# Kernel optimization log

Hardware: AMD Instinct MI355X
Metric: run time of the kernel (lower is better)

Reference implementation:

```python
import jax, jax.numpy as jnp
import numpy as np

B, H, W, DIM = 8, 128, 128, 96
MED = 2 * DIM            # med_channels
NS = 3                   # num_scales
SCTX = 48                # spatial context channels
RIN = DIM + SCTX         # reweight mlp input
RHID = int(0.25 * RIN)   # 36
ROUT = NS * MED          # 576
FH, FWH = H, W // 2 + 1  # rfft2 output grid
SCALE_HW = [(16, 9), (8, 4), (24, 13)]  # per-scale filter resolutions


def _cubic(t, a=-0.75):
    t = abs(t)
    if t <= 1.0:
        return (a + 2) * t ** 3 - (a + 3) * t ** 2 + 1.0
    if t < 2.0:
        return a * t ** 3 - 5 * a * t ** 2 + 8 * a * t - 4 * a
    return 0.0


def _resize_mat(old, new):
    # bicubic, align_corners=True, border replication (matches F.interpolate)
    M = np.zeros((new, old), dtype=np.float32)
    for j in range(new):
        s = j * (old - 1) / (new - 1) if new > 1 else 0.0
        f = int(np.floor(s))
        for k in range(-1, 3):
            M[j, min(max(f + k, 0), old - 1)] += _cubic(s - (f + k))
    return jnp.asarray(M)


def _soa(x, scale, bias):
    r = jnp.maximum(x, 0.0)
    return scale * r * r + bias


def setup_inputs() -> dict:
    key = jax.random.key(0)
    ks = jax.random.split(key, 10)
    inp = {
        "x": jax.random.normal(ks[0], (B, H, W, DIM), dtype=jnp.float32),
        "w1": jax.random.normal(ks[1], (MED, DIM), dtype=jnp.float32) * 0.02,
        "soa1_scale": jnp.ones((1,), jnp.float32),
        "soa1_bias": jnp.zeros((1,), jnp.float32),
        "cw0": jax.random.normal(ks[2], (SCALE_HW[0][0], SCALE_HW[0][1], MED, 2), dtype=jnp.float32) * 0.02,
        "cw1": jax.random.normal(ks[3], (SCALE_HW[1][0], SCALE_HW[1][1], MED, 2), dtype=jnp.float32) * 0.02,
        "cw2": jax.random.normal(ks[4], (SCALE_HW[2][0], SCALE_HW[2][1], MED, 2), dtype=jnp.float32) * 0.02,
        "sp_w": jax.random.normal(ks[5], (SCTX, DIM), dtype=jnp.float32) * 0.05,
        "bn_gamma": jnp.ones((SCTX,), jnp.float32),
        "bn_beta": jnp.zeros((SCTX,), jnp.float32),
        "bn_mean": jnp.zeros((SCTX,), jnp.float32),
        "bn_var": jnp.ones((SCTX,), jnp.float32),
        "fc1": jax.random.normal(ks[6], (RHID, RIN), dtype=jnp.float32) * 0.05,
        "mlp_scale": jnp.ones((1,), jnp.float32),
        "mlp_bias": jnp.zeros((1,), jnp.float32),
        "fc2": jax.random.normal(ks[7], (ROUT, RHID), dtype=jnp.float32) * 0.05,
        "w2": jax.random.normal(ks[8], (DIM, MED), dtype=jnp.float32) * 0.02,
    }
    return inp


def reference(x, w1, soa1_scale, soa1_bias, cw0, cw1, cw2, sp_w,
              bn_gamma, bn_beta, bn_mean, bn_var,
              fc1, mlp_scale, mlp_bias, fc2, w2):
    # pwconv1 + Soa act
    x_pre = _soa(jnp.einsum('bhwc,mc->bhwm', x, w1), soa1_scale, soa1_bias)
    # rfft2 over spatial dims (ortho) -> [B, FH, FWH, MED] complex64
    xf = jnp.fft.rfft2(x_pre.transpose(0, 3, 1, 2), axes=(2, 3), norm='ortho').transpose(0, 2, 3, 1)
    # resize each scale's complex weight to the fft grid (bicubic align_corners=True)
    filts = []
    for cw in (cw0, cw1, cw2):
        Rh = _resize_mat(cw.shape[0], FH)
        Rw = _resize_mat(cw.shape[1], FWH)
        t = jnp.einsum('Hh,hwmc->Hwmc', Rh, cw)
        t = jnp.einsum('Ww,Hwmc->HWmc', Rw, t)
        filts.append(jax.lax.complex(t[..., 0], t[..., 1]))
    filt = jnp.stack(filts)  # [NS, FH, FWH, MED] complex64
    # routing context: global channel mean + 1x1 conv / BN(eval) / relu / GAP
    gctx = x.mean(axis=(1, 2))  # [B, DIM]
    y = jnp.einsum('bhwc,sc->bhws', x, sp_w)
    y = (y - bn_mean) * jax.lax.rsqrt(bn_var + 1e-5) * bn_gamma + bn_beta
    sctx = jnp.maximum(y, 0.0).mean(axis=(1, 2))  # [B, SCTX]
    fused = jnp.concatenate([gctx, sctx], axis=1)  # [B, RIN]
    hmid = _soa(fused @ fc1.T, mlp_scale, mlp_bias)
    r = jax.nn.softmax((hmid @ fc2.T).reshape(-1, NS, MED), axis=1)  # [B, NS, MED]
    # routing-weighted combined filter + spectral multiply
    comb = jnp.einsum('shwm,bsm->bhwm', filt, r.astype(filt.dtype))
    xff = xf * comb
    xsp = jnp.fft.irfft2(xff.transpose(0, 3, 1, 2), s=(H, W), axes=(2, 3), norm='ortho').transpose(0, 2, 3, 1)
    # act2 is Identity; pwconv2
    return jnp.einsum('bhwm,cm->bhwc', xsp, w2)
```

## Files before the change

kernel.cpp:

```cpp
#include <hip/hip_runtime.h>
#include <math.h>

#define BB    8
#define HH    128
#define WW    128
#define DIM   96
#define MED   192
#define HWPX  16384
#define FWH   65
#define LSTR  67

#define P_OFF     0
#define P_SZ      (8*192*16384)
#define FILT_OFF  (P_OFF + P_SZ)
#define FILT_SZ   (3*192*128*65*2)
#define GS_OFF    (FILT_OFF + FILT_SZ)
#define SS_OFF    (GS_OFF + 768)
#define R_OFF     (SS_OFF + 384)
#define W1B_OFF   (R_OFF + 4608)
#define W2B_OFF   (W1B_OFF + 23040)

typedef __attribute__((ext_vector_type(8))) short short8_t;
typedef __attribute__((ext_vector_type(4))) float float4_t;

__device__ __forceinline__ unsigned short bf16_rne(float f){
  unsigned u = __float_as_uint(f);
  unsigned r = (u + 0x7FFFu + ((u>>16)&1u)) >> 16;
  return (unsigned short)r;
}
__device__ __forceinline__ float bf16_to_f(unsigned short h){
  return __uint_as_float(((unsigned)h) << 16);
}

__global__ __launch_bounds__(256) void k_prep(
    const float* __restrict__ w1, const float* __restrict__ sp_w,
    const float* __restrict__ w2,
    unsigned short* __restrict__ W1B, unsigned short* __restrict__ W2B)
{
  int tid = threadIdx.x + blockIdx.x*256;
  int nthr = 256*36;
  for (int i = tid; i < 2*3*15*512; i += nthr) {
    int j = i & 7, l = (i>>3) & 63;
    int nt = (i>>9) % 15, kc = ((i>>9)/15) % 3, term = i / (3*15*512);
    int r = nt*16 + (l&15);
    int c = kc*32 + (l>>4)*8 + j;
    float v = (r < 192) ? w1[r*96 + c] : sp_w[(r-192)*96 + c];
    unsigned short hi = bf16_rne(v);
    W1B[i] = (term==0) ? hi : bf16_rne(v - bf16_to_f(hi));
  }
  for (int i = tid; i < 2*6*6*512; i += nthr) {
    int j = i & 7, l = (i>>3) & 63;
    int nt = (i>>9) % 6, kc = ((i>>9)/6) % 6, term = i / (6*6*512);
    int cp = nt*16 + (l&15);
    int m  = kc*32 + (l>>4)*8 + j;
    float v = w2[cp*192 + m];
    unsigned short hi = bf16_rne(v);
    W2B[i] = (term==0) ? hi : bf16_rne(v - bf16_to_f(hi));
  }
}

__global__ __launch_bounds__(256) void k_pw1(
    const float* __restrict__ x, const unsigned short* __restrict__ W1B,
    const float* __restrict__ soa_scale, const float* __restrict__ soa_bias,
    const float* __restrict__ bn_gamma, const float* __restrict__ bn_beta,
    const float* __restrict__ bn_mean, const float* __restrict__ bn_var,
    float* __restrict__ P, float* __restrict__ gsum, float* __restrict__ ssum)
{
  __shared__ float red[4][144];
  __shared__ float bnA_s[48], bnB_s[48];
  int t = threadIdx.x;
  int lane = t & 63, wv = t >> 6;
  if (t < 48) {
    float a = bn_gamma[t] * rsqrtf(bn_var[t] + 1e-5f);
    bnA_s[t] = a; bnB_s[t] = bn_beta[t] - bn_mean[t]*a;
  }
  int px0 = blockIdx.x*64 + wv*16;
  int b = (blockIdx.x*64) >> 14;
  int pxl = px0 & 16383;
  int g = lane >> 4;

  float4_t acc[15];
  #pragma unroll
  for (int nt=0; nt<15; ++nt) acc[nt] = (float4_t){0.f,0.f,0.f,0.f};

  #pragma unroll
  for (int kc=0; kc<3; ++kc) {
    const float* xp = x + (size_t)(px0 + (lane&15))*96 + kc*32 + g*8;
    float4 v0 = *(const float4*)xp;
    float4 v1 = *(const float4*)(xp+4);
    float vv[8] = {v0.x,v0.y,v0.z,v0.w, v1.x,v1.y,v1.z,v1.w};
    #pragma unroll
    for (int j=0;j<8;j++){
      float s = vv[j];
      s += __shfl_xor(s, 1);
      s += __shfl_xor(s, 2);
      s += __shfl_xor(s, 4);
      s += __shfl_xor(s, 8);
      if ((lane & 15) == 0) red[wv][kc*32 + g*8 + j] = s;
    }
    short8_t Bh, Bl;
    #pragma unroll
    for (int j=0;j<8;j++){
      unsigned short h = bf16_rne(vv[j]);
      Bh[j] = (short)h;
      Bl[j] = (short)bf16_rne(vv[j] - bf16_to_f(h));
    }
    const short8_t* a_hi = (const short8_t*)(W1B + (size_t)(0*3+kc)*15*512) + lane;
    const short8_t* a_lo = (const short8_t*)(W1B + (size_t)(1*3+kc)*15*512) + lane;
    #pragma unroll
    for (int nt=0; nt<15; ++nt) {
      short8_t Ah = a_hi[nt*64];
      short8_t Al = a_lo[nt*64];
      acc[nt] = __builtin_amdgcn_mfma_f32_16x16x32_bf16(Ah, Bh, acc[nt], 0,0,0);
      acc[nt] = __builtin_amdgcn_mfma_f32_16x16x32_bf16(Ah, Bl, acc[nt], 0,0,0);
      acc[nt] = __builtin_amdgcn_mfma_f32_16x16x32_bf16(Al, Bh, acc[nt], 0,0,0);
    }
  }
  float sc = soa_scale[0], bi = soa_bias[0];
  #pragma unroll
  for (int nt=0; nt<12; ++nt) {
    #pragma unroll
    for (int q=0;q<4;q++){
      float d = acc[nt][q];
      float v = fmaxf(d, 0.f);
      d = sc*v*v + bi;
      int mp = nt*16 + g*4 + q;
      P[(size_t)(b*192 + mp)*HWPX + pxl + (lane&15)] = d;
    }
  }
  #pragma unroll
  for (int tile=0; tile<3; ++tile) {
    #pragma unroll
    for (int q=0;q<4;q++){
      int s = tile*16 + g*4 + q;
      float y = acc[12+tile][q];
      float v = fmaxf(bnA_s[s]*y + bnB_s[s], 0.f);
      v += __shfl_xor(v, 1);
      v += __shfl_xor(v, 2);
      v += __shfl_xor(v, 4);
      v += __shfl_xor(v, 8);
      if ((lane & 15) == 0) red[wv][96 + s] = v;
    }
  }
  __syncthreads();
  if (t < 144) {
    float s = red[0][t] + red[1][t] + red[2][t] + red[3][t];
    if (t < 96) atomicAdd(&gsum[b*96 + t], s);
    else        atomicAdd(&ssum[b*48 + (t-96)], s);
  }
}

__global__ __launch_bounds__(256) void k_pw2(
    const float* __restrict__ P, const unsigned short* __restrict__ W2B,
    float* __restrict__ out)
{
  int t = threadIdx.x;
  int lane = t & 63, wv = t >> 6;
  int px0 = blockIdx.x*64 + wv*16;
  int b = px0 >> 14;
  int pxl = px0 & 16383;

  float4_t acc[6];
  #pragma unroll
  for (int nt=0; nt<6; ++nt) acc[nt] = (float4_t){0.f,0.f,0.f,0.f};

  #pragma unroll
  for (int kc=0; kc<6; ++kc) {
    const float* ap = P + (size_t)(b*192 + kc*32 + (lane>>4)*8)*HWPX + pxl + (lane&15);
    short8_t Ah, Al;
    #pragma unroll
    for (int j=0;j<8;j++){
      float v = ap[(size_t)j*HWPX];
      unsigned short h = bf16_rne(v);
      Ah[j] = (short)h;
      Al[j] = (short)bf16_rne(v - bf16_to_f(h));
    }
    const short8_t* b_hi = (const short8_t*)(W2B + (size_t)(0*6+kc)*6*512) + lane;
    const short8_t* b_lo = (const short8_t*)(W2B + (size_t)(1*6+kc)*6*512) + lane;
    #pragma unroll
    for (int nt=0; nt<6; ++nt) {
      short8_t Bh = b_hi[nt*64];
      short8_t Bl = b_lo[nt*64];
      acc[nt] = __builtin_amdgcn_mfma_f32_16x16x32_bf16(Ah, Bh, acc[nt], 0,0,0);
      acc[nt] = __builtin_amdgcn_mfma_f32_16x16x32_bf16(Ah, Bl, acc[nt], 0,0,0);
      acc[nt] = __builtin_amdgcn_mfma_f32_16x16x32_bf16(Al, Bh, acc[nt], 0,0,0);
    }
  }
  #pragma unroll
  for (int nt=0; nt<6; ++nt) {
    #pragma unroll
    for (int q=0;q<4;q++){
      int px = px0 + (lane>>4)*4 + q;
      out[(size_t)px*96 + nt*16 + (lane&15)] = acc[nt][q];
    }
  }
}

__global__ __launch_bounds__(256) void k_route2(
    const float* __restrict__ gsum, const float* __restrict__ ssum,
    const float* __restrict__ fc1, const float* __restrict__ fc2,
    const float* __restrict__ mlp_scale, const float* __restrict__ mlp_bias,
    float* __restrict__ r_out)
{
  __shared__ float fused[144], hmid[36], rpre[576];
  int t = threadIdx.x, b = blockIdx.x;
  if (t < 96) fused[t] = gsum[b*96+t] * (1.f/16384.f);
  else if (t < 144) fused[t] = ssum[b*48 + (t-96)] * (1.f/16384.f);
  __syncthreads();
  if (t < 36) {
    float a = 0.f;
    for (int i=0;i<144;i++) a = fmaf(fused[i], fc1[t*144+i], a);
    float rr = fmaxf(a, 0.f);
    hmid[t] = mlp_scale[0]*rr*rr + mlp_bias[0];
  }
  __syncthreads();
  for (int o = t; o < 576; o += 256) {
    float a = 0.f;
    for (int j=0;j<36;j++) a = fmaf(hmid[j], fc2[o*36+j], a);
    rpre[o] = a;
  }
  __syncthreads();
  if (t < 192) {
    float v0 = rpre[t], v1 = rpre[192+t], v2 = rpre[384+t];
    float mx = fmaxf(v0, fmaxf(v1, v2));
    float e0 = expf(v0-mx), e1 = expf(v1-mx), e2 = expf(v2-mx);
    float inv = 1.f/(e0+e1+e2);
    r_out[(b*3+0)*192+t] = e0*inv;
    r_out[(b*3+1)*192+t] = e1*inv;
    r_out[(b*3+2)*192+t] = e2*inv;
  }
}

__device__ __forceinline__ float cubicw(float tt){
  float t = fabsf(tt), t2=t*t, t3=t2*t;
  if (t <= 1.f) return 1.25f*t3 - 2.25f*t2 + 1.f;
  if (t < 2.f)  return -0.75f*t3 + 3.75f*t2 - 6.f*t + 3.f;
  return 0.f;
}

__global__ __launch_bounds__(256) void k_filt(
    const float* __restrict__ cw0, const float* __restrict__ cw1,
    const float* __restrict__ cw2, float* __restrict__ filt)
{
  int bx = blockIdx.x; int s = bx >> 7; int fh = bx & 127;
  const float* cw = (s==0) ? cw0 : ((s==1) ? cw1 : cw2);
  int SH = (s==0) ? 16 : ((s==1) ? 8 : 24);
  int SW = (s==0) ? 9  : ((s==1) ? 4 : 13);
  float sh = fh * (float)(SH-1) / 127.f;
  int fh0 = (int)floorf(sh);
  float wh[4]; int ih[4];
  #pragma unroll
  for (int k=0;k<4;k++){
    int kk = fh0-1+k;
    wh[k] = cubicw(sh - (float)kk);
    ih[k] = min(max(kk,0), SH-1);
  }
  int t = threadIdx.x;
  for (int i = t; i < 192*65; i += 256) {
    int m = i / 65, fw = i % 65;
    float sw = fw * (float)(SW-1) / 64.f;
    int fw0 = (int)floorf(sw);
    float are=0.f, aim=0.f;
    #pragma unroll
    for (int kb=0;kb<4;kb++){
      int jj = fw0-1+kb;
      float wwb = cubicw(sw - (float)jj);
      int iw = min(max(jj,0), SW-1);
      #pragma unroll
      for (int ka=0;ka<4;ka++){
        const float* p = cw + (size_t)((ih[ka]*SW + iw)*192 + m)*2;
        float wgt = wh[ka]*wwb;
        are = fmaf(wgt, p[0], are);
        aim = fmaf(wgt, p[1], aim);
      }
    }
    *(float2*)&filt[ (size_t)(((s*192+m)*128 + fh)*65 + fw) * 2 ] = make_float2(are, aim);
  }
}

__device__ __forceinline__ float2 c_add(float2 a, float2 b){ return make_float2(a.x+b.x, a.y+b.y); }
__device__ __forceinline__ float2 c_sub(float2 a, float2 b){ return make_float2(a.x-b.x, a.y-b.y); }
__device__ __forceinline__ float2 c_mul(float2 a, float2 w){ return make_float2(a.x*w.x - a.y*w.y, a.x*w.y + a.y*w.x); }
__device__ __forceinline__ float2 c_mulc(float2 a, float2 w){ return make_float2(a.x*w.x + a.y*w.y, a.y*w.x - a.x*w.y); }

__device__ __forceinline__ void dif4(float2* S, const float2* TW,
    int a0, int a1, int a2, int a3, int t1, int t2, int t3)
{
  float2 x0=S[a0], x1=S[a1], x2=S[a2], x3=S[a3];
  float2 u = c_add(x0,x2), d0 = c_sub(x0,x2);
  float2 s = c_add(x1,x3), d1 = c_sub(x1,x3);
  float2 w = c_mul(d0, TW[t1]);
  float2 v = c_mul(d1, TW[t2]);
  float2 t3w = TW[t3];
  S[a0] = c_add(u,s);
  S[a1] = c_mul(c_sub(u,s), t3w);
  S[a2] = c_add(w,v);
  S[a3] = c_mul(c_sub(w,v), t3w);
}

__device__ __forceinline__ void dit4(float2* S, const float2* TW,
    int a0, int a1, int a2, int a3, int tA, int tB, int tC)
{
  float2 x0=S[a0], x1=S[a1], x2=S[a2], x3=S[a3];
  float2 wA = TW[tA];
  float2 x1t = c_mulc(x1, wA), x3t = c_mulc(x3, wA);
  float2 u = c_add(x0,x1t), v = c_sub(x0,x1t);
  float2 s = c_add(x2,x3t), w = c_sub(x2,x3t);
  float2 st = c_mulc(s, TW[tB]);
  float2 wt = c_mulc(w, TW[tC]);
  S[a0] = c_add(u, st);
  S[a2] = c_sub(u, st);
  S[a1] = c_add(v, wt);
  S[a3] = c_sub(v, wt);
}

__global__ __launch_bounds__(512, 4) void k_spectral(
    float* __restrict__ P, const float* __restrict__ filt, const float* __restrict__ r)
{
  __shared__ float2 S[128*LSTR];
  __shared__ float2 TW[64];
  int t = threadIdx.x;
  int bm = blockIdx.x;
  int b = bm & 7; int m = bm >> 3;
  float* plane = P + ((size_t)b*192 + m) * HWPX;

  if (t < 64) {
    float ang = -6.283185307179586477f * (float)t / 128.f;
    TW[t] = make_float2(cosf(ang), sinf(ang));
  }
  for (int it = 0; it < 8; ++it) {
    int idx = t + 512*it;
    int h = idx >> 5, j = idx & 31;
    float4 v = ((const float4*)plane)[idx];
    int base = h*LSTR + 2*j;
    S[base]   = make_float2(v.x, v.y);
    S[base+1] = make_float2(v.z, v.w);
  }
  float r0 = r[(b*3+0)*192+m];
  float r1 = r[(b*3+1)*192+m];
  float r2 = r[(b*3+2)*192+m];
  __syncthreads();

  #pragma unroll
  for (int ps = 0; ps < 3; ++ps) {
    const int lh = 5 - 2*ps;
    const int h1 = 1 << lh, h2 = h1 >> 1;
    for (int it = 0; it < 4; ++it) {
      int idx = t + 512*it;
      int g = idx & 15, row = idx >> 4;
      int k = g & (h2-1), blk = g >> (lh-1);
      int base = row*LSTR + blk*(2*h1) + k;
      dif4(S,TW, base, base+h2, base+h1, base+h1+h2,
           k << (6-lh), (k+h2) << (6-lh), k << (7-lh));
    }
    __syncthreads();
  }

  for (int it = 0; it < 9; ++it) {
    int idx = t + 512*it;
    if (idx < 128*33) {
      int row = idx & 127, k = idx >> 7;
      int base = row*LSTR;
      if (k == 0) {
        float2 z = S[base];
        S[base]    = make_float2(z.x + z.y, 0.f);
        S[base+64] = make_float2(z.x - z.y, 0.f);
      } else {
        int a = __brev((unsigned)k) >> 26;
        int bidx = __brev((unsigned)(64-k)) >> 26;
        float2 A = S[base+a], B = S[base+bidx];
        float sr_ = 0.5f*(A.x+B.x), si_ = 0.5f*(A.y-B.y);
        float dr  = 0.5f*(A.x-B.x), di  = 0.5f*(A.y+B.y);
        float2 w = TW[k];
        float tr = w.x*di + w.y*dr;
        float ti = -(w.x*dr - w.y*di);
        S[base+a]    = make_float2(sr_ + tr,  si_ + ti);
        S[base+bidx] = make_float2(sr_ - tr, -si_ + ti);
      }
    }
  }
  __syncthreads();

  #pragma unroll
  for (int ps = 0; ps < 3; ++ps) {
    const int lh = 6 - 2*ps;
    const int h1 = 1 << lh, h2 = h1 >> 1;
    for (int it = 0; it < 5; ++it) {
      int idx = t + 512*it;
      if (idx < 65*32) {
        int g = idx / 65, col = idx - g*65;
        int k = g & (h2-1), blk = g >> (lh-1);
        int p = blk*(2*h1) + k;
        dif4(S,TW, p*LSTR+col, (p+h2)*LSTR+col, (p+h1)*LSTR+col, (p+h1+h2)*LSTR+col,
             k << (6-lh), (k+h2) << (6-lh), k << (7-lh));
      }
    }
    __syncthreads();
  }
  for (int it = 0; it < 9; ++it) {
    int idx = t + 512*it;
    if (idx < 65*64) {
      int j = idx / 65, col = idx - j*65;
      int a0 = (2*j)*LSTR + col, a1 = a0 + LSTR;
      float2 u = S[a0], v = S[a1];
      S[a0] = c_add(u,v); S[a1] = c_sub(u,v);
    }
  }
  __syncthreads();

  {
    const float2* fb0 = (const float2*)filt + (size_t)(0*192+m)*8320;
    const float2* fb1 = (const float2*)filt + (size_t)(1*192+m)*8320;
    const float2* fb2 = (const float2*)filt + (size_t)(2*192+m)*8320;
    const float inv = 1.f/8192.f;
    for (int it = 0; it < 17; ++it) {
      int idx = t + 512*it;
      if (idx < 8320) {
        int fh = idx / 65, fw = idx - fh*65;
        float2 f0 = fb0[idx], f1 = fb1[idx], f2 = fb2[idx];
        float cr = (r0*f0.x + r1*f1.x + r2*f2.x) * inv;
        float ci = (r0*f0.y + r1*f1.y + r2*f2.y) * inv;
        int sh = __brev((unsigned)fh) >> 25;
        int sw = (fw == 64) ? 64 : (__brev((unsigned)fw) >> 26);
        int a = sh*LSTR + sw;
        float2 X = S[a];
        S[a] = make_float2(X.x*cr - X.y*ci, X.x*ci + X.y*cr);
      }
    }
  }
  __syncthreads();

  #pragma unroll
  for (int ps = 0; ps < 3; ++ps) {
    const int la = 2*ps;
    const int h = 1 << la;
    for (int it = 0; it < 5; ++it) {
      int idx = t + 512*it;
      if (idx < 65*32) {
        int g = idx / 65, col = idx - g*65;
        int k = g & (h-1), blk = g >> la;
        int p = blk*(4*h) + k;
        dit4(S,TW, p*LSTR+col, (p+h)*LSTR+col, (p+2*h)*LSTR+col, (p+3*h)*LSTR+col,
             k << (6-la), k << (5-la), (k+h) << (5-la));
      }
    }
    __syncthreads();
  }
  for (int it = 0; it < 9; ++it) {
    int idx = t + 512*it;
    if (idx < 65*64) {
      int k = idx / 65, col = idx - k*65;
      int a0 = k*LSTR + col, a1 = a0 + 64*LSTR;
      float2 u = S[a0], xv = S[a1];
      float2 xt = c_mulc(xv, TW[k]);
      S[a0] = c_add(u,xt); S[a1] = c_sub(u,xt);
    }
  }
  __syncthreads();

  for (int it = 0; it < 9; ++it) {
    int idx = t + 512*it;
    if (idx < 128*33) {
      int row = idx & 127, k = idx >> 7;
      int base = row*LSTR;
      if (k == 0) {
        float ar = S[base].x;
        float cr = S[base+64].x;
        S[base] = make_float2(0.5f*(ar+cr), 0.5f*(ar-cr));
      } else {
        int a = __brev((unsigned)k) >> 26;
        int bidx = __brev((unsigned)(64-k)) >> 26;
        float2 A = S[base+a], B = S[base+bidx];
        float sr_ = 0.5f*(A.x+B.x), si_ = 0.5f*(A.y-B.y);
        float dr  = 0.5f*(A.x-B.x), di  = 0.5f*(A.y+B.y);
        float2 w = TW[k];
        float tr2 = w.y*dr - w.x*di;
        float ti2 = w.x*dr + w.y*di;
        S[base+a]    = make_float2(sr_ + tr2,  si_ + ti2);
        S[base+bidx] = make_float2(sr_ - tr2, -si_ + ti2);
      }
    }
  }
  __syncthreads();

  #pragma unroll
  for (int ps = 0; ps < 3; ++ps) {
    const int la = 2*ps;
    const int h = 1 << la;
    for (int it = 0; it < 4; ++it) {
      int idx = t + 512*it;
      int g = idx & 15, row = idx >> 4;
      int k = g & (h-1), blk = g >> la;
      int base = row*LSTR + blk*(4*h) + k;
      dit4(S,TW, base, base+h, base+2*h, base+3*h,
           k << (6-la), k << (5-la), (k+h) << (5-la));
    }
    __syncthreads();
  }

  for (int it = 0; it < 8; ++it) {
    int idx = t + 512*it;
    int h = idx >> 5, j = idx & 31;
    int base = h*LSTR + 2*j;
    float2 z0 = S[base], z1 = S[base+1];
    float4 v; v.x = z0.x; v.y = z0.y; v.z = z1.x; v.w = z1.y;
    ((float4*)plane)[idx] = v;
  }
}

extern "C" void kernel_launch(void* const* d_in, const int* in_sizes, int n_in,
                              void* d_out, int out_size, void* d_ws, size_t ws_size,
                              hipStream_t stream) {
  const float* x          = (const float*)d_in[0];
  const float* w1         = (const float*)d_in[1];
  const float* soa1_scale = (const float*)d_in[2];
  const float* soa1_bias  = (const float*)d_in[3];
  const float* cw0        = (const float*)d_in[4];
  const float* cw1        = (const float*)d_in[5];
  const float* cw2        = (const float*)d_in[6];
  const float* sp_w       = (const float*)d_in[7];
  const float* bn_gamma   = (const float*)d_in[8];
  const float* bn_beta    = (const float*)d_in[9];
  const float* bn_mean    = (const float*)d_in[10];
  const float* bn_var     = (const float*)d_in[11];
  const float* fc1        = (const float*)d_in[12];
  const float* mlp_scale  = (const float*)d_in[13];
  const float* mlp_bias   = (const float*)d_in[14];
  const float* fc2        = (const float*)d_in[15];
  const float* w2         = (const float*)d_in[16];
  float* out = (float*)d_out;

  float* ws   = (float*)d_ws;
  float* P    = ws + P_OFF;
  float* filt = ws + FILT_OFF;
  float* gsum = ws + GS_OFF;
  float* ssum = ws + SS_OFF;
  float* rbuf = ws + R_OFF;
  unsigned short* W1B = (unsigned short*)(ws + W1B_OFF);
  unsigned short* W2B = (unsigned short*)(ws + W2B_OFF);

  hipMemsetAsync(gsum, 0, (768+384)*sizeof(float), stream);

  k_prep   <<<36,   256, 0, stream>>>(w1, sp_w, w2, W1B, W2B);
  k_pw1    <<<2048, 256, 0, stream>>>(x, W1B, soa1_scale, soa1_bias,
                                      bn_gamma, bn_beta, bn_mean, bn_var,
                                      P, gsum, ssum);
  k_route2 <<<8,    256, 0, stream>>>(gsum, ssum, fc1, fc2, mlp_scale, mlp_bias, rbuf);
  k_filt   <<<384,  256, 0, stream>>>(cw0, cw1, cw2, filt);
  k_spectral<<<1536,512, 0, stream>>>(P, filt, rbuf);
  k_pw2    <<<2048, 256, 0, stream>>>(P, W2B, out);
}
```

Baseline: 419.7 us.

## Merge setup kernels and fold routing MLP into last pw1 block

Filter interpolation, weight packing and the accumulator zeroing are merged into a single setup kernel, which replaces a memset and two separate launches. The routing MLP now runs inside the final k_pw1 block, found through an atomic completion counter, which removes the k_route2 launch. k_spectral's block-to-(batch, channel) mapping changes so consecutive blocks walk channels within one batch. The cost is a serial tail in which one block computes the MLP for all 8 batches while the rest of the GPU sits idle.

```diff
diff --git a/kernel.cpp b/kernel.cpp
--- a/kernel.cpp
+++ b/kernel.cpp
@@ -1,13 +1,7 @@
 #include <hip/hip_runtime.h>
 #include <math.h>
 
-#define BB    8
-#define HH    128
-#define WW    128
-#define DIM   96
-#define MED   192
 #define HWPX  16384
-#define FWH   65
 #define LSTR  67
 
 #define P_OFF     0
@@ -16,7 +10,8 @@
 #define FILT_SZ   (3*192*128*65*2)
 #define GS_OFF    (FILT_OFF + FILT_SZ)
 #define SS_OFF    (GS_OFF + 768)
-#define R_OFF     (SS_OFF + 384)
+#define CNT_OFF   (SS_OFF + 384)
+#define R_OFF     (CNT_OFF + 8)
 #define W1B_OFF   (R_OFF + 4608)
 #define W2B_OFF   (W1B_OFF + 23040)
 
@@ -32,30 +27,82 @@
   return __uint_as_float(((unsigned)h) << 16);
 }
 
-__global__ __launch_bounds__(256) void k_prep(
+__device__ __forceinline__ float cubicw(float tt){
+  float t = fabsf(tt), t2=t*t, t3=t2*t;
+  if (t <= 1.f) return 1.25f*t3 - 2.25f*t2 + 1.f;
+  if (t < 2.f)  return -0.75f*t3 + 3.75f*t2 - 6.f*t + 3.f;
+  return 0.f;
+}
+
+__global__ __launch_bounds__(256) void k_setup(
     const float* __restrict__ w1, const float* __restrict__ sp_w,
     const float* __restrict__ w2,
-    unsigned short* __restrict__ W1B, unsigned short* __restrict__ W2B)
+    const float* __restrict__ cw0, const float* __restrict__ cw1,
+    const float* __restrict__ cw2,
+    unsigned short* __restrict__ W1B, unsigned short* __restrict__ W2B,
+    float* __restrict__ filt, float* __restrict__ zero_base)
 {
-  int tid = threadIdx.x + blockIdx.x*256;
-  int nthr = 256*36;
-  for (int i = tid; i < 2*3*15*512; i += nthr) {
-    int j = i & 7, l = (i>>3) & 63;
-    int nt = (i>>9) % 15, kc = ((i>>9)/15) % 3, term = i / (3*15*512);
-    int r = nt*16 + (l&15);
-    int c = kc*32 + (l>>4)*8 + j;
-    float v = (r < 192) ? w1[r*96 + c] : sp_w[(r-192)*96 + c];
-    unsigned short hi = bf16_rne(v);
-    W1B[i] = (term==0) ? hi : bf16_rne(v - bf16_to_f(hi));
-  }
-  for (int i = tid; i < 2*6*6*512; i += nthr) {
-    int j = i & 7, l = (i>>3) & 63;
-    int nt = (i>>9) % 6, kc = ((i>>9)/6) % 6, term = i / (6*6*512);
-    int cp = nt*16 + (l&15);
-    int m  = kc*32 + (l>>4)*8 + j;
-    float v = w2[cp*192 + m];
-    unsigned short hi = bf16_rne(v);
-    W2B[i] = (term==0) ? hi : bf16_rne(v - bf16_to_f(hi));
+  int bx = blockIdx.x;
+  int t = threadIdx.x;
+  if (bx < 1536) {
+    int s = bx >> 9; int idx = bx & 511; int fh = idx >> 2; int mq = idx & 3;
+    const float* cw = (s==0) ? cw0 : ((s==1) ? cw1 : cw2);
+    int SH = (s==0) ? 16 : ((s==1) ? 8 : 24);
+    int SW = (s==0) ? 9  : ((s==1) ? 4 : 13);
+    float sh = fh * (float)(SH-1) / 127.f;
+    int fh0 = (int)floorf(sh);
+    float wh[4]; int ih[4];
+    #pragma unroll
+    for (int k=0;k<4;k++){
+      int kk = fh0-1+k;
+      wh[k] = cubicw(sh - (float)kk);
+      ih[k] = min(max(kk,0), SH-1);
+    }
+    for (int i = t; i < 48*65; i += 256) {
+      int m = mq*48 + i/65, fw = i%65;
+      float sw = fw * (float)(SW-1) / 64.f;
+      int fw0 = (int)floorf(sw);
+      float are=0.f, aim=0.f;
+      #pragma unroll
+      for (int kb=0;kb<4;kb++){
+        int jj = fw0-1+kb;
+        float wwb = cubicw(sw - (float)jj);
+        int iw = min(max(jj,0), SW-1);
+        #pragma unroll
+        for (int ka=0;ka<4;ka++){
+          const float* p = cw + (size_t)((ih[ka]*SW + iw)*192 + m)*2;
+          float wgt = wh[ka]*wwb;
+          are = fmaf(wgt, p[0], are);
+          aim = fmaf(wgt, p[1], aim);
+        }
+      }
+      *(float2*)&filt[ (size_t)(((s*192+m)*128 + fh)*65 + fw) * 2 ] = make_float2(are, aim);
+    }
+  } else {
+    int pbx = bx - 1536;
+    if (pbx == 0) {
+      for (int i = t; i < 768+384+8; i += 256) zero_base[i] = 0.f;
+    }
+    int tid = t + pbx*256;
+    int nthr = 256*36;
+    for (int i = tid; i < 2*3*15*512; i += nthr) {
+      int j = i & 7, l = (i>>3) & 63;
+      int nt = (i>>9) % 15, kc = ((i>>9)/15) % 3, term = i / (3*15*512);
+      int r = nt*16 + (l&15);
+      int c = kc*32 + (l>>4)*8 + j;
+      float v = (r < 192) ? w1[r*96 + c] : sp_w[(r-192)*96 + c];
+      unsigned short hi = bf16_rne(v);
+      W1B[i] = (term==0) ? hi : bf16_rne(v - bf16_to_f(hi));
+    }
+    for (int i = tid; i < 2*6*6*512; i += nthr) {
+      int j = i & 7, l = (i>>3) & 63;
+      int nt = (i>>9) % 6, kc = ((i>>9)/6) % 6, term = i / (6*6*512);
+      int cp = nt*16 + (l&15);
+      int mm = kc*32 + (l>>4)*8 + j;
+      float v = w2[cp*192 + mm];
+      unsigned short hi = bf16_rne(v);
+      W2B[i] = (term==0) ? hi : bf16_rne(v - bf16_to_f(hi));
+    }
   }
 }
 
@@ -64,10 +111,14 @@
     const float* __restrict__ soa_scale, const float* __restrict__ soa_bias,
     const float* __restrict__ bn_gamma, const float* __restrict__ bn_beta,
     const float* __restrict__ bn_mean, const float* __restrict__ bn_var,
-    float* __restrict__ P, float* __restrict__ gsum, float* __restrict__ ssum)
+    const float* __restrict__ fc1, const float* __restrict__ fc2,
+    const float* __restrict__ mlp_scale, const float* __restrict__ mlp_bias,
+    float* __restrict__ P, float* __restrict__ gsum, float* __restrict__ ssum,
+    float* __restrict__ rbuf, unsigned int* __restrict__ cnt)
 {
   __shared__ float red[4][144];
   __shared__ float bnA_s[48], bnB_s[48];
+  __shared__ int lastFlag;
   int t = threadIdx.x;
   int lane = t & 63, wv = t >> 6;
   if (t < 48) {
@@ -148,133 +199,45 @@
     if (t < 96) atomicAdd(&gsum[b*96 + t], s);
     else        atomicAdd(&ssum[b*48 + (t-96)], s);
   }
-}
-
-__global__ __launch_bounds__(256) void k_pw2(
-    const float* __restrict__ P, const unsigned short* __restrict__ W2B,
-    float* __restrict__ out)
-{
-  int t = threadIdx.x;
-  int lane = t & 63, wv = t >> 6;
-  int px0 = blockIdx.x*64 + wv*16;
-  int b = px0 >> 14;
-  int pxl = px0 & 16383;
-
-  float4_t acc[6];
-  #pragma unroll
-  for (int nt=0; nt<6; ++nt) acc[nt] = (float4_t){0.f,0.f,0.f,0.f};
-
-  #pragma unroll
-  for (int kc=0; kc<6; ++kc) {
-    const float* ap = P + (size_t)(b*192 + kc*32 + (lane>>4)*8)*HWPX + pxl + (lane&15);
-    short8_t Ah, Al;
-    #pragma unroll
-    for (int j=0;j<8;j++){
-      float v = ap[(size_t)j*HWPX];
-      unsigned short h = bf16_rne(v);
-      Ah[j] = (short)h;
-      Al[j] = (short)bf16_rne(v - bf16_to_f(h));
-    }
-    const short8_t* b_hi = (const short8_t*)(W2B + (size_t)(0*6+kc)*6*512) + lane;
-    const short8_t* b_lo = (const short8_t*)(W2B + (size_t)(1*6+kc)*6*512) + lane;
-    #pragma unroll
-    for (int nt=0; nt<6; ++nt) {
-      short8_t Bh = b_hi[nt*64];
-      short8_t Bl = b_lo[nt*64];
-      acc[nt] = __builtin_amdgcn_mfma_f32_16x16x32_bf16(Ah, Bh, acc[nt], 0,0,0);
-      acc[nt] = __builtin_amdgcn_mfma_f32_16x16x32_bf16(Ah, Bl, acc[nt], 0,0,0);
-      acc[nt] = __builtin_amdgcn_mfma_f32_16x16x32_bf16(Al, Bh, acc[nt], 0,0,0);
-    }
-  }
-  #pragma unroll
-  for (int nt=0; nt<6; ++nt) {
-    #pragma unroll
-    for (int q=0;q<4;q++){
-      int px = px0 + (lane>>4)*4 + q;
-      out[(size_t)px*96 + nt*16 + (lane&15)] = acc[nt][q];
-    }
-  }
-}
-
-__global__ __launch_bounds__(256) void k_route2(
-    const float* __restrict__ gsum, const float* __restrict__ ssum,
-    const float* __restrict__ fc1, const float* __restrict__ fc2,
-    const float* __restrict__ mlp_scale, const float* __restrict__ mlp_bias,
-    float* __restrict__ r_out)
-{
+  __threadfence();
+  __syncthreads();
+  if (t == 0) {
+    unsigned int old = atomicAdd(cnt, 1u);
+    lastFlag = (old == 2047u) ? 1 : 0;
+  }
+  __syncthreads();
+  if (!lastFlag) return;
+  __threadfence();
+
   __shared__ float fused[144], hmid[36], rpre[576];
-  int t = threadIdx.x, b = blockIdx.x;
-  if (t < 96) fused[t] = gsum[b*96+t] * (1.f/16384.f);
-  else if (t < 144) fused[t] = ssum[b*48 + (t-96)] * (1.f/16384.f);
-  __syncthreads();
-  if (t < 36) {
-    float a = 0.f;
-    for (int i=0;i<144;i++) a = fmaf(fused[i], fc1[t*144+i], a);
-    float rr = fmaxf(a, 0.f);
-    hmid[t] = mlp_scale[0]*rr*rr + mlp_bias[0];
-  }
-  __syncthreads();
-  for (int o = t; o < 576; o += 256) {
-    float a = 0.f;
-    for (int j=0;j<36;j++) a = fmaf(hmid[j], fc2[o*36+j], a);
-    rpre[o] = a;
-  }
-  __syncthreads();
-  if (t < 192) {
-    float v0 = rpre[t], v1 = rpre[192+t], v2 = rpre[384+t];
-    float mx = fmaxf(v0, fmaxf(v1, v2));
-    float e0 = expf(v0-mx), e1 = expf(v1-mx), e2 = expf(v2-mx);
-    float inv = 1.f/(e0+e1+e2);
-    r_out[(b*3+0)*192+t] = e0*inv;
-    r_out[(b*3+1)*192+t] = e1*inv;
-    r_out[(b*3+2)*192+t] = e2*inv;
-  }
-}
-
-__device__ __forceinline__ float cubicw(float tt){
-  float t = fabsf(tt), t2=t*t, t3=t2*t;
-  if (t <= 1.f) return 1.25f*t3 - 2.25f*t2 + 1.f;
-  if (t < 2.f)  return -0.75f*t3 + 3.75f*t2 - 6.f*t + 3.f;
-  return 0.f;
-}
-
-__global__ __launch_bounds__(256) void k_filt(
-    const float* __restrict__ cw0, const float* __restrict__ cw1,
-    const float* __restrict__ cw2, float* __restrict__ filt)
-{
-  int bx = blockIdx.x; int s = bx >> 7; int fh = bx & 127;
-  const float* cw = (s==0) ? cw0 : ((s==1) ? cw1 : cw2);
-  int SH = (s==0) ? 16 : ((s==1) ? 8 : 24);
-  int SW = (s==0) ? 9  : ((s==1) ? 4 : 13);
-  float sh = fh * (float)(SH-1) / 127.f;
-  int fh0 = (int)floorf(sh);
-  float wh[4]; int ih[4];
-  #pragma unroll
-  for (int k=0;k<4;k++){
-    int kk = fh0-1+k;
-    wh[k] = cubicw(sh - (float)kk);
-    ih[k] = min(max(kk,0), SH-1);
-  }
-  int t = threadIdx.x;
-  for (int i = t; i < 192*65; i += 256) {
-    int m = i / 65, fw = i % 65;
-    float sw = fw * (float)(SW-1) / 64.f;
-    int fw0 = (int)floorf(sw);
-    float are=0.f, aim=0.f;
-    #pragma unroll
-    for (int kb=0;kb<4;kb++){
-      int jj = fw0-1+kb;
-      float wwb = cubicw(sw - (float)jj);
-      int iw = min(max(jj,0), SW-1);
-      #pragma unroll
-      for (int ka=0;ka<4;ka++){
-        const float* p = cw + (size_t)((ih[ka]*SW + iw)*192 + m)*2;
-        float wgt = wh[ka]*wwb;
-        are = fmaf(wgt, p[0], are);
-        aim = fmaf(wgt, p[1], aim);
-      }
-    }
-    *(float2*)&filt[ (size_t)(((s*192+m)*128 + fh)*65 + fw) * 2 ] = make_float2(are, aim);
+  float msc = mlp_scale[0], mbi = mlp_bias[0];
+  for (int bb = 0; bb < 8; ++bb) {
+    if (t < 96)       fused[t] = atomicAdd(&gsum[bb*96 + t], 0.f) * (1.f/16384.f);
+    else if (t < 144) fused[t] = atomicAdd(&ssum[bb*48 + (t-96)], 0.f) * (1.f/16384.f);
+    __syncthreads();
+    if (t < 36) {
+      float a = 0.f;
+      for (int i=0;i<144;i++) a = fmaf(fused[i], fc1[t*144+i], a);
+      float rr = fmaxf(a, 0.f);
+      hmid[t] = msc*rr*rr + mbi;
+    }
+    __syncthreads();
+    for (int o = t; o < 576; o += 256) {
+      float a = 0.f;
+      for (int j=0;j<36;j++) a = fmaf(hmid[j], fc2[o*36+j], a);
+      rpre[o] = a;
+    }
+    __syncthreads();
+    if (t < 192) {
+      float v0 = rpre[t], v1 = rpre[192+t], v2 = rpre[384+t];
+      float mx = fmaxf(v0, fmaxf(v1, v2));
+      float e0 = expf(v0-mx), e1 = expf(v1-mx), e2 = expf(v2-mx);
+      float inv = 1.f/(e0+e1+e2);
+      rbuf[(bb*3+0)*192+t] = e0*inv;
+      rbuf[(bb*3+1)*192+t] = e1*inv;
+      rbuf[(bb*3+2)*192+t] = e2*inv;
+    }
+    __syncthreads();
   }
 }
 
@@ -321,7 +284,7 @@
   __shared__ float2 TW[64];
   int t = threadIdx.x;
   int bm = blockIdx.x;
-  int b = bm & 7; int m = bm >> 3;
+  int b = bm / 192; int m = bm % 192;
   float* plane = P + ((size_t)b*192 + m) * HWPX;
 
   if (t < 64) {
@@ -508,6 +471,52 @@
   }
 }
 
+__global__ __launch_bounds__(256) void k_pw2(
+    const float* __restrict__ P, const unsigned short* __restrict__ W2B,
+    float* __restrict__ out)
+{
+  int t = threadIdx.x;
+  int lane = t & 63, wv = t >> 6;
+  int px0 = blockIdx.x*64 + wv*16;
+  int b = px0 >> 14;
+  int pxl = px0 & 16383;
+
+  float4_t acc[6];
+  #pragma unroll
+  for (int nt=0; nt<6; ++nt) acc[nt] = (float4_t){0.f,0.f,0.f,0.f};
+
+  #pragma unroll
+  for (int kc=0; kc<6; ++kc) {
+    const float* ap = P + (size_t)(b*192 + kc*32 + (lane>>4)*8)*HWPX + pxl + (lane&15);
+    short8_t Ah, Al;
+    #pragma unroll
+    for (int j=0;j<8;j++){
+      float v = ap[(size_t)j*HWPX];
+      unsigned short h = bf16_rne(v);
+      Ah[j] = (short)h;
+      Al[j] = (short)bf16_rne(v - bf16_to_f(h));
+    }
+    const short8_t* b_hi = (const short8_t*)(W2B + (size_t)(0*6+kc)*6*512) + lane;
+    const short8_t* b_lo = (const short8_t*)(W2B + (size_t)(1*6+kc)*6*512) + lane;
+    #pragma unroll
+    for (int nt=0; nt<6; ++nt) {
+      short8_t Bh = b_hi[nt*64];
+      short8_t Bl = b_lo[nt*64];
+      acc[nt] = __builtin_amdgcn_mfma_f32_16x16x32_bf16(Ah, Bh, acc[nt], 0,0,0);
+      acc[nt] = __builtin_amdgcn_mfma_f32_16x16x32_bf16(Ah, Bl, acc[nt], 0,0,0);
+      acc[nt] = __builtin_amdgcn_mfma_f32_16x16x32_bf16(Al, Bh, acc[nt], 0,0,0);
+    }
+  }
+  #pragma unroll
+  for (int nt=0; nt<6; ++nt) {
+    #pragma unroll
+    for (int q=0;q<4;q++){
+      int px = px0 + (lane>>4)*4 + q;
+      out[(size_t)px*96 + nt*16 + (lane&15)] = acc[nt][q];
+    }
+  }
+}
+
 extern "C" void kernel_launch(void* const* d_in, const int* in_sizes, int n_in,
                               void* d_out, int out_size, void* d_ws, size_t ws_size,
                               hipStream_t stream) {
@@ -536,17 +545,15 @@
   float* gsum = ws + GS_OFF;
   float* ssum = ws + SS_OFF;
   float* rbuf = ws + R_OFF;
+  unsigned int* cnt = (unsigned int*)(ws + CNT_OFF);
   unsigned short* W1B = (unsigned short*)(ws + W1B_OFF);
   unsigned short* W2B = (unsigned short*)(ws + W2B_OFF);
 
-  hipMemsetAsync(gsum, 0, (768+384)*sizeof(float), stream);
-
-  k_prep   <<<36,   256, 0, stream>>>(w1, sp_w, w2, W1B, W2B);
+  k_setup  <<<1572, 256, 0, stream>>>(w1, sp_w, w2, cw0, cw1, cw2, W1B, W2B, filt, gsum);
   k_pw1    <<<2048, 256, 0, stream>>>(x, W1B, soa1_scale, soa1_bias,
                                       bn_gamma, bn_beta, bn_mean, bn_var,
-                                      P, gsum, ssum);
-  k_route2 <<<8,    256, 0, stream>>>(gsum, ssum, fc1, fc2, mlp_scale, mlp_bias, rbuf);
-  k_filt   <<<384,  256, 0, stream>>>(cw0, cw1, cw2, filt);
+                                      fc1, fc2, mlp_scale, mlp_bias,
+                                      P, gsum, ssum, rbuf, cnt);
   k_spectral<<<1536,512, 0, stream>>>(P, filt, rbuf);
   k_pw2    <<<2048, 256, 0, stream>>>(P, W2B, out);
 }
```

After: 616.1 us. +46.8%, slower.
